# Performance work log

Measured on AMD Instinct MI355X. Metric: run time of the kernel, lower is better.

## Reference

```python
import jax, jax.numpy as jnp
import numpy as np

EMBED_DIM = 1024
NUM_HEADS = 16
HEAD_DIM = EMBED_DIM // NUM_HEADS
SCALING = HEAD_DIM ** -0.5
NEG_FILL = -1e30


def setup_inputs() -> dict:
    key = jax.random.key(0)
    k1, k2, k3 = jax.random.split(key, 3)
    T, B, E = 2048, 4, EMBED_DIM
    query = jax.random.normal(k1, (T, B, E), dtype=jnp.float32)
    key_padding_mask = jnp.zeros((B, T), dtype=bool)  # 1 = padded key
    # xavier_uniform-like init
    lim_in = (6.0 / (3 * E + E)) ** 0.5
    in_proj_weight = jax.random.uniform(k2, (3 * E, E), minval=-lim_in, maxval=lim_in, dtype=jnp.float32)
    in_proj_bias = jnp.zeros((3 * E,), dtype=jnp.float32)
    lim_out = (6.0 / (E + E)) ** 0.5
    out_w = jax.random.uniform(k3, (E, E), minval=-lim_out, maxval=lim_out, dtype=jnp.float32)
    out_b = jnp.zeros((E,), dtype=jnp.float32)
    return {"query": query, "key_padding_mask": key_padding_mask,
            "in_proj_weight": in_proj_weight, "in_proj_bias": in_proj_bias,
            "out_w": out_w, "out_b": out_b}


def reference(query, key_padding_mask, in_proj_weight, in_proj_bias, out_w, out_b):
    T, B, E = query.shape
    H, D = NUM_HEADS, HEAD_DIM
    # fused in-projection (self-attention: qkv from same input)
    qkv = query @ in_proj_weight.T + in_proj_bias  # [T,B,3E]
    q, k, v = jnp.split(qkv, 3, axis=-1)
    q = q * SCALING
    q = q.reshape(T, B, H, D)
    k = k.reshape(T, B, H, D)
    v = v.reshape(T, B, H, D)
    # attention scores [B,H,T,S]
    scores = jnp.einsum('tbhd,sbhd->bhts', q, k)
    scores = jnp.where(key_padding_mask[:, None, None, :], NEG_FILL, scores)
    attn_w = jax.nn.softmax(scores, axis=-1)  # [B,H,T,S]
    # weighted sum of values -> [T,B,E]
    attn = jnp.einsum('bhts,sbhd->tbhd', attn_w, v).reshape(T, B, E)
    attn = attn @ out_w.T + out_b
    attn_w_avg = jnp.sum(attn_w, axis=1) / H  # [B,T,S]
    return attn, attn_w_avg
```

## Files before the change

### kernel.cpp

```cpp
#include <hip/hip_runtime.h>
#include <stdint.h>

#define QSCALE 0.18033688011112042f

typedef unsigned short u16;
typedef unsigned int u32;
typedef unsigned long long u64;
typedef _Float16 f16;
typedef __attribute__((ext_vector_type(2))) __fp16 h16x2;
typedef __attribute__((ext_vector_type(8))) _Float16 f16x8;
typedef __attribute__((ext_vector_type(8))) __bf16 bf16x8;
typedef __attribute__((ext_vector_type(4))) float f32x4;
typedef __attribute__((ext_vector_type(16))) float f32x16;
typedef __attribute__((ext_vector_type(8))) u16 u16x8;
typedef __attribute__((ext_vector_type(4))) u32 u32x4;

__device__ __forceinline__ void gl_lds16(const void* g, void* l) {
  __builtin_amdgcn_global_load_lds(
      (const __attribute__((address_space(1))) void*)g,
      (__attribute__((address_space(3))) void*)l, 16, 0, 0);
}

__device__ __forceinline__ u16 f2bf(float f) {
  unsigned int u = __float_as_uint(f);
  u += 0x7FFFu + ((u >> 16) & 1u);
  return (u16)(u >> 16);
}

extern "C" __global__ __launch_bounds__(256) void cvt_all(
    const float* __restrict__ query, const float* __restrict__ w_in,
    const float* __restrict__ w_out, u16* __restrict__ dst) {
  int i = (blockIdx.x * 256 + threadIdx.x) * 4;
  const float* src;
  int off;
  if (i < 8388608) {
    src = query; off = i;
  } else if (i < 11534336) {
    src = w_in; off = i - 8388608;
  } else {
    src = w_out; off = i - 11534336;
  }
  float4 v = *(const float4*)(src + off);
  ushort4 o;
  o.x = f2bf(v.x); o.y = f2bf(v.y); o.z = f2bf(v.z); o.w = f2bf(v.w);
  *(ushort4*)(dst + i) = o;
}

extern "C" __global__ __launch_bounds__(128) void mask_bits(
    const unsigned char* __restrict__ mask, u64* __restrict__ mbits) {
  const int i = threadIdx.x;
  const unsigned char* p = mask + i * 64;
  u64 bits = 0;
#pragma unroll
  for (int j = 0; j < 8; ++j) {
    const u64 c = *(const u64*)(p + j * 8);
#pragma unroll
    for (int bb = 0; bb < 8; ++bb)
      if ((c >> (8 * bb)) & 0xFFull) bits |= 1ull << (j * 8 + bb);
  }
  mbits[i] = bits;
}

extern "C" __global__ __launch_bounds__(256) void gemm_qkv(
    const u16* __restrict__ X, const u16* __restrict__ W,
    const float* __restrict__ bias,
    u16* __restrict__ qb, u16* __restrict__ kb, u16* __restrict__ vb) {
  const int tid = threadIdx.x;
  const int w = tid >> 6, lane = tid & 63;
  const int lg = lane >> 4, ll = lane & 15;
  const int wm = w >> 1, wn = w & 1;
  const int row0A = blockIdx.x * 128;
  const int row0B = blockIdx.y * 128;

  __shared__ __align__(16) u16 As[2][128 * 32];
  __shared__ __align__(16) u16 Bs[2][128 * 32];

  f32x4 acc[4][4] = {};

  const int r_st = tid >> 2;
  const int cb_st = (tid & 3) * 16;

#pragma unroll
  for (int it = 0; it < 2; ++it) {
    gl_lds16((const char*)X + ((size_t)(row0A + it * 64 + r_st) * 1024) * 2 + cb_st,
             (char*)&As[0][0] + it * 4096 + w * 1024);
    gl_lds16((const char*)W + ((size_t)(row0B + it * 64 + r_st) * 1024) * 2 + cb_st,
             (char*)&Bs[0][0] + it * 4096 + w * 1024);
  }

  for (int kt = 0; kt < 32; ++kt) {
    const int cur = kt & 1;
    asm volatile("s_waitcnt vmcnt(0)" ::: "memory");
    __syncthreads();
    if (kt + 1 < 32) {
      const int k0 = (kt + 1) * 32;
#pragma unroll
      for (int it = 0; it < 2; ++it) {
        gl_lds16((const char*)X + ((size_t)(row0A + it * 64 + r_st) * 1024 + k0) * 2 + cb_st,
                 (char*)&As[cur ^ 1][0] + it * 4096 + w * 1024);
        gl_lds16((const char*)W + ((size_t)(row0B + it * 64 + r_st) * 1024 + k0) * 2 + cb_st,
                 (char*)&Bs[cur ^ 1][0] + it * 4096 + w * 1024);
      }
    }
    const u16* Ab = &As[cur][0];
    const u16* Bb = &Bs[cur][0];
    const int kc = lg * 8;
    bf16x8 a[4], bfr[4];
#pragma unroll
    for (int i = 0; i < 4; ++i)
      a[i] = *(const bf16x8*)(Ab + (wm * 64 + i * 16 + ll) * 32 + kc);
#pragma unroll
    for (int j = 0; j < 4; ++j)
      bfr[j] = *(const bf16x8*)(Bb + (wn * 64 + j * 16 + ll) * 32 + kc);
#pragma unroll
    for (int i = 0; i < 4; ++i)
#pragma unroll
      for (int j = 0; j < 4; ++j)
        acc[i][j] = __builtin_amdgcn_mfma_f32_16x16x32_bf16(a[i], bfr[j], acc[i][j], 0, 0, 0);
  }

  const int which = row0B >> 10;
  if (which == 2) {
#pragma unroll
    for (int j = 0; j < 4; ++j) {
      const int n = row0B + wn * 64 + j * 16 + ll;
      const float bv = bias[n];
      const int n2 = n & 1023;
      const int hh = n2 >> 6, dd = n2 & 63;
#pragma unroll
      for (int i = 0; i < 4; ++i)
#pragma unroll
        for (int r = 0; r < 4; ++r) {
          const int m = row0A + wm * 64 + i * 16 + lg * 4 + r;
          const int tt = m >> 2, bb = m & 3;
          const f16 hv = (f16)(acc[i][j][r] + bv);
          vb[((size_t)(bb * 16 + hh) * 2048 + tt) * 64 + dd] =
              __builtin_bit_cast(u16, hv);
        }
    }
  } else {
    u16* dst = which == 0 ? qb : kb;
    const float scl = which == 0 ? QSCALE : 1.0f;
#pragma unroll
    for (int j = 0; j < 4; ++j) {
      const int n = row0B + wn * 64 + j * 16 + ll;
      const float bv = bias[n];
      const int n2 = n & 1023;
      const int hh = n2 >> 6, dd = n2 & 63;
#pragma unroll
      for (int i = 0; i < 4; ++i)
#pragma unroll
        for (int r = 0; r < 4; ++r) {
          const int m = row0A + wm * 64 + i * 16 + lg * 4 + r;
          const int tt = m >> 2, bb = m & 3;
          dst[((size_t)(bb * 16 + hh) * 2048 + tt) * 64 + dd] =
              f2bf((acc[i][j][r] + bv) * scl);
        }
    }
  }
}

extern "C" __global__ __launch_bounds__(256) void transpose_v(
    const u16* __restrict__ v, u16* __restrict__ vt) {
  const int blk = blockIdx.x;
  const int bh = blk >> 5, tt = blk & 31;
  const int t0 = tt * 64;
  const int tid = threadIdx.x;
  __shared__ __align__(16) u16 tile[64][72];
  const u16* src = v + ((size_t)bh * 2048 + t0) * 64;
#pragma unroll
  for (int it = 0; it < 2; ++it) {
    const int r = it * 32 + (tid >> 3);
    const int c = (tid & 7) * 8;
    *(u16x8*)(&tile[r][c]) = *(const u16x8*)(src + (size_t)r * 64 + c);
  }
  __syncthreads();
  u16* dstb = vt + (size_t)bh * 64 * 2048 + t0;
#pragma unroll
  for (int it = 0; it < 2; ++it) {
    const int d = it * 32 + (tid >> 3);
    const int s = (tid & 7) * 8;
    u16x8 o;
#pragma unroll
    for (int jj = 0; jj < 8; ++jj) o[jj] = tile[s + jj][d];
    *(u16x8*)(dstb + (size_t)d * 2048 + s) = o;
  }
}

extern "C" __global__ __launch_bounds__(256, 4) void flash_fwd(
    const u16* __restrict__ q, const u16* __restrict__ k,
    const u16* __restrict__ vt, const u64* __restrict__ mbits,
    u16* __restrict__ attn_pre, float* __restrict__ stat_il) {
  const int lb = ((blockIdx.x & 7) << 7) + (blockIdx.x >> 3);
  const int bh = lb >> 4, tt = lb & 15;
  const int b = bh >> 4, hd = bh & 15;
  const int t0 = tt * 128;
  const int tid = threadIdx.x, w = tid >> 6, lane = tid & 63;
  const int hl = lane >> 5;
  const int l31 = lane & 31;

  __shared__ __align__(16) u16 Ks[2][64 * 64];
  __shared__ __align__(16) u16 Vs[2][64 * 64];

  const int qrow = t0 + w * 32 + l31;
  const u16* qp = q + ((size_t)bh * 2048 + qrow) * 64 + hl * 8;
  bf16x8 qreg[4];
#pragma unroll
  for (int kg = 0; kg < 4; ++kg) qreg[kg] = *(const bf16x8*)(qp + kg * 16);

  f32x16 po[2] = {};
  float ls0 = 0.f, ls1 = 0.f;
  const h16x2 ones = {(__fp16)1.0f, (__fp16)1.0f};

  const int slot_r = tid >> 3;
  const int slot_c8 = (tid & 7) ^ (slot_r & 7);

#define STAGE_F(buf, s0_)                                                      \
  do {                                                                         \
    _Pragma("unroll") for (int it2 = 0; it2 < 2; ++it2) {                      \
      const int rr = it2 * 32 + slot_r;                                        \
      gl_lds16((const char*)k +                                                \
                   (((size_t)bh * 2048 + (s0_) + rr) * 64 + slot_c8 * 8) * 2,  \
               (char*)&Ks[buf][0] + it2 * 4096 + w * 1024);                    \
      gl_lds16((const char*)vt +                                               \
                   (((size_t)bh * 64 + rr) * 2048 + (s0_) + slot_c8 * 8) * 2,  \
               (char*)&Vs[buf][0] + it2 * 4096 + w * 1024);                    \
    }                                                                          \
  } while (0)

  STAGE_F(0, 0);
  asm volatile("s_waitcnt vmcnt(0)" ::: "memory");
  __builtin_amdgcn_s_barrier();

  for (int t = 0; t < 32; ++t) {
    const u64 mb = mbits[b * 32 + t];
    const int cur = t & 1;
    if (t + 1 < 32) STAGE_F(cur ^ 1, (t + 1) * 64);

    const char* Kb = (const char*)&Ks[cur][0];
    const char* Vb = (const char*)&Vs[cur][0];

#pragma unroll
    for (int kt = 0; kt < 2; ++kt) {
      f32x16 z = {};
      const int key = kt * 32 + l31;
      __builtin_amdgcn_s_setprio(1);
#pragma unroll
      for (int kg = 0; kg < 4; ++kg) {
        const bf16x8 kf = *(const bf16x8*)(
            Kb + key * 128 + ((((kg << 1) | hl) ^ (key & 7)) << 4));
        z = __builtin_amdgcn_mfma_f32_32x32x16_bf16(kf, qreg[kg], z, 0, 0, 0);
      }
      __builtin_amdgcn_s_setprio(0);

      float ps[16];
#pragma unroll
      for (int r = 0; r < 16; ++r) ps[r] = __builtin_amdgcn_exp2f(z[r]);
      const u32 m32 = (u32)(mb >> (kt * 32));
      if (m32) {
#pragma unroll
        for (int r = 0; r < 16; ++r) {
          const int bitpos = (r & 3) + 8 * (r >> 2) + 4 * hl;
          if ((m32 >> bitpos) & 1u) ps[r] = 0.f;
        }
      }

      u32 w8[8];
#pragma unroll
      for (int j = 0; j < 8; ++j) {
        const h16x2 pk = __builtin_amdgcn_cvt_pkrtz(ps[2 * j], ps[2 * j + 1]);
        w8[j] = __builtin_bit_cast(u32, pk);
        if (j & 1)
          ls1 = __builtin_amdgcn_fdot2(pk, ones, ls1, false);
        else
          ls0 = __builtin_amdgcn_fdot2(pk, ones, ls0, false);
      }

#pragma unroll
      for (int f = 0; f < 2; ++f) {
        u32 d0 = w8[4 * f], d1 = w8[4 * f + 1];
        u32 s0w = w8[4 * f + 2], s1w = w8[4 * f + 3];
        asm volatile("v_permlane32_swap_b32 %0, %1" : "+v"(d0), "+v"(s0w));
        asm volatile("v_permlane32_swap_b32 %0, %1" : "+v"(d1), "+v"(s1w));
        const f16x8 pa = __builtin_bit_cast(f16x8, (u32x4){d0, d1, s0w, s1w});
        const int g = kt * 2 + f;
        __builtin_amdgcn_s_setprio(1);
#pragma unroll
        for (int dt = 0; dt < 2; ++dt) {
          const int d = dt * 32 + l31;
          const f16x8 vf = *(const f16x8*)(
              Vb + d * 128 + ((((g << 1) | hl) ^ (d & 7)) << 4));
          po[dt] = __builtin_amdgcn_mfma_f32_32x32x16_f16(pa, vf, po[dt], 0, 0, 0);
        }
        __builtin_amdgcn_s_setprio(0);
      }
    }

    asm volatile("s_waitcnt vmcnt(0)" ::: "memory");
    __builtin_amdgcn_s_barrier();
  }

  float lsum = ls0 + ls1;
  lsum += __shfl_xor(lsum, 32, 64);
  const float linv = 1.0f / lsum;
  if (lane < 32)
    stat_il[(size_t)bh * 2048 + t0 + w * 32 + lane] = linv;

#pragma unroll
  for (int r = 0; r < 16; ++r) {
    const int qi = (r & 3) + 8 * (r >> 2) + 4 * hl;
    const float lv = __shfl(linv, qi, 64);
    const int trow = t0 + w * 32 + qi;
#pragma unroll
    for (int dt = 0; dt < 2; ++dt) {
      const int dd = dt * 32 + l31;
      attn_pre[((size_t)(trow * 4 + b)) * 1024 + hd * 64 + dd] =
          f2bf(po[dt][r] * lv);
    }
  }
#undef STAGE_F
}

extern "C" __global__ __launch_bounds__(256, 3) void wavg(
    const u16* __restrict__ q, const u16* __restrict__ k,
    const u64* __restrict__ mbits,
    const float* __restrict__ stat_il, float* __restrict__ wout) {
  const int lb = ((blockIdx.x & 7) << 8) + (blockIdx.x >> 3);
  const int b = lb >> 9, tt = (lb >> 5) & 15, st = lb & 31;
  const int t0 = tt * 128, s0 = st * 64;
  const int tid = threadIdx.x, w = tid >> 6, lane = tid & 63;
  const int hl = lane >> 5;
  const int l31 = lane & 31;

  __shared__ __align__(16) u16 Qs[2][128 * 64];
  __shared__ __align__(16) u16 Ks2[2][64 * 64];

  const int slot_r8 = tid >> 3;
  const int slot_c8 = (tid & 7) ^ (slot_r8 & 7);

  const u64 mbw = mbits[b * 32 + st];
  const u32 m32lo = (u32)mbw, m32hi = (u32)(mbw >> 32);
  const bool domask = mbw != 0ull;

#define STAGE_W(buf, hh)                                                       \
  do {                                                                         \
    const size_t qo_ = (size_t)(b * 16 + (hh)) * 2048;                         \
    _Pragma("unroll") for (int i2 = 0; i2 < 4; ++i2) {                         \
      const int rr = i2 * 32 + slot_r8;                                        \
      gl_lds16((const char*)q + ((qo_ + t0 + rr) * 64 + slot_c8 * 8) * 2,      \
               (char*)&Qs[buf][0] + i2 * 4096 + w * 1024);                     \
    }                                                                          \
    _Pragma("unroll") for (int i2 = 0; i2 < 2; ++i2) {                         \
      const int rr = i2 * 32 + slot_r8;                                        \
      gl_lds16((const char*)k + ((qo_ + s0 + rr) * 64 + slot_c8 * 8) * 2,      \
               (char*)&Ks2[buf][0] + i2 * 4096 + w * 1024);                    \
    }                                                                          \
  } while (0)

  STAGE_W(0, 0);
  asm volatile("s_waitcnt vmcnt(0)" ::: "memory");
  __syncthreads();

  float accw[32] = {};
  for (int h = 0; h < 16; ++h) {
    const int cur = h & 1;
    const float ilh =
        stat_il[(size_t)(b * 16 + h) * 2048 + t0 + w * 32 + l31];

    if (h + 1 < 16) STAGE_W(cur ^ 1, h + 1);

    const char* Qb = (const char*)&Qs[cur][0];
    const char* Kb = (const char*)&Ks2[cur][0];

    const int qr = w * 32 + l31;
    bf16x8 qf[4];
#pragma unroll
    for (int kg = 0; kg < 4; ++kg)
      qf[kg] = *(const bf16x8*)(
          Qb + qr * 128 + ((((kg << 1) | hl) ^ (qr & 7)) << 4));

    f32x16 z0 = {}, z1 = {};
    __builtin_amdgcn_s_setprio(1);
#pragma unroll
    for (int kg = 0; kg < 4; ++kg) {
      const int key = l31;
      const bf16x8 kf = *(const bf16x8*)(
          Kb + key * 128 + ((((kg << 1) | hl) ^ (key & 7)) << 4));
      z0 = __builtin_amdgcn_mfma_f32_32x32x16_bf16(kf, qf[kg], z0, 0, 0, 0);
    }
#pragma unroll
    for (int kg = 0; kg < 4; ++kg) {
      const int key = 32 + l31;
      const bf16x8 kf = *(const bf16x8*)(
          Kb + key * 128 + ((((kg << 1) | hl) ^ (key & 7)) << 4));
      z1 = __builtin_amdgcn_mfma_f32_32x32x16_bf16(kf, qf[kg], z1, 0, 0, 0);
    }
    __builtin_amdgcn_s_setprio(0);

#pragma unroll
    for (int r = 0; r < 16; ++r) {
      float p = __builtin_amdgcn_exp2f(z0[r]);
      if (domask) {
        const int bitpos = (r & 3) + 8 * (r >> 2) + 4 * hl;
        if ((m32lo >> bitpos) & 1u) p = 0.f;
      }
      accw[r] = fmaf(p, ilh, accw[r]);
    }
#pragma unroll
    for (int r = 0; r < 16; ++r) {
      float p = __builtin_amdgcn_exp2f(z1[r]);
      if (domask) {
        const int bitpos = (r & 3) + 8 * (r >> 2) + 4 * hl;
        if ((m32hi >> bitpos) & 1u) p = 0.f;
      }
      accw[16 + r] = fmaf(p, ilh, accw[16 + r]);
    }

    asm volatile("s_waitcnt vmcnt(0)" ::: "memory");
    __syncthreads();
  }

  float* tb = ((float*)&Qs[0][0]) + w * 2048;
#pragma unroll
  for (int kt = 0; kt < 2; ++kt)
#pragma unroll
    for (int j = 0; j < 4; ++j) {
      f32x4 qd;
#pragma unroll
      for (int e = 0; e < 4; ++e) qd[e] = accw[kt * 16 + 4 * j + e] * 0.0625f;
      const int slot = kt * 8 + 2 * j + hl;
      *(f32x4*)(tb + l31 * 64 + ((slot ^ (l31 & 7)) << 2)) = qd;
    }
  __syncthreads();
#pragma unroll
  for (int j2 = 0; j2 < 8; ++j2) {
    const int row = j2 * 4 + (lane >> 4);
    const int slot = lane & 15;
    const f32x4 v = *(const f32x4*)(tb + row * 64 + ((slot ^ (row & 7)) << 2));
    *(f32x4*)(wout + ((size_t)b * 2048 + t0 + w * 32 + row) * 2048 + s0 +
              slot * 4) = v;
  }
#undef STAGE_W
}

extern "C" __global__ __launch_bounds__(256) void gemm_out(
    const u16* __restrict__ A, const u16* __restrict__ W,
    const float* __restrict__ bias, float* __restrict__ out) {
  const int tid = threadIdx.x;
  const int w = tid >> 6, lane = tid & 63;
  const int lg = lane >> 4, ll = lane & 15;
  const int wm = w >> 1, wn = w & 1;
  const int row0A = blockIdx.x * 128;
  const int row0B = blockIdx.y * 128;

  __shared__ __align__(16) u16 As[2][128 * 32];
  __shared__ __align__(16) u16 Bs[2][128 * 32];

  f32x4 acc[4][4] = {};
  const int r_st = tid >> 2;
  const int cb_st = (tid & 3) * 16;

#pragma unroll
  for (int it = 0; it < 2; ++it) {
    gl_lds16((const char*)A + ((size_t)(row0A + it * 64 + r_st) * 1024) * 2 + cb_st,
             (char*)&As[0][0] + it * 4096 + w * 1024);
    gl_lds16((const char*)W + ((size_t)(row0B + it * 64 + r_st) * 1024) * 2 + cb_st,
             (char*)&Bs[0][0] + it * 4096 + w * 1024);
  }

  for (int kt = 0; kt < 32; ++kt) {
    const int cur = kt & 1;
    asm volatile("s_waitcnt vmcnt(0)" ::: "memory");
    __syncthreads();
    if (kt + 1 < 32) {
      const int k0 = (kt + 1) * 32;
#pragma unroll
      for (int it = 0; it < 2; ++it) {
        gl_lds16((const char*)A + ((size_t)(row0A + it * 64 + r_st) * 1024 + k0) * 2 + cb_st,
                 (char*)&As[cur ^ 1][0] + it * 4096 + w * 1024);
        gl_lds16((const char*)W + ((size_t)(row0B + it * 64 + r_st) * 1024 + k0) * 2 + cb_st,
                 (char*)&Bs[cur ^ 1][0] + it * 4096 + w * 1024);
      }
    }
    const u16* Ab = &As[cur][0];
    const u16* Bb = &Bs[cur][0];
    const int kc = lg * 8;
    bf16x8 a[4], bfr[4];
#pragma unroll
    for (int i = 0; i < 4; ++i)
      a[i] = *(const bf16x8*)(Ab + (wm * 64 + i * 16 + ll) * 32 + kc);
#pragma unroll
    for (int j = 0; j < 4; ++j)
      bfr[j] = *(const bf16x8*)(Bb + (wn * 64 + j * 16 + ll) * 32 + kc);
#pragma unroll
    for (int i = 0; i < 4; ++i)
#pragma unroll
      for (int j = 0; j < 4; ++j)
        acc[i][j] = __builtin_amdgcn_mfma_f32_16x16x32_bf16(a[i], bfr[j], acc[i][j], 0, 0, 0);
  }

#pragma unroll
  for (int j = 0; j < 4; ++j) {
    const int n = row0B + wn * 64 + j * 16 + ll;
    const float bv = bias[n];
#pragma unroll
    for (int i = 0; i < 4; ++i)
#pragma unroll
      for (int r = 0; r < 4; ++r) {
        const int m = row0A + wm * 64 + i * 16 + lg * 4 + r;
        out[(size_t)m * 1024 + n] = acc[i][j][r] + bv;
      }
  }
}

extern "C" void kernel_launch(void* const* d_in, const int* in_sizes, int n_in,
                              void* d_out, int out_size, void* d_ws, size_t ws_size,
                              hipStream_t stream) {
  const float* query = (const float*)d_in[0];
  const unsigned char* mask = (const unsigned char*)d_in[1];
  const float* w_in = (const float*)d_in[2];
  const float* b_in = (const float*)d_in[3];
  const float* w_out = (const float*)d_in[4];
  const float* b_out = (const float*)d_in[5];

  float* out0 = (float*)d_out;
  float* outw = out0 + (size_t)8388608;

  char* ws = (char*)d_ws;
  u16* Xbf   = (u16*)(ws + 0);
  u16* Wqkv  = (u16*)(ws + 16777216);
  u16* Woutb = (u16*)(ws + 23068672);
  u16* qb    = (u16*)(ws + 25165824);
  u16* kb    = (u16*)(ws + 41943040);
  u16* vb    = (u16*)(ws + 58720256);
  u16* vtb   = (u16*)(ws + 75497472);
  u16* ap    = (u16*)(ws + 92274688);
  float* sil = (float*)(ws + 109051904);
  u64* mbits = (u64*)(ws + 109576192);

  cvt_all<<<12288, 256, 0, stream>>>(query, w_in, w_out, Xbf);
  mask_bits<<<1, 128, 0, stream>>>(mask, mbits);
  gemm_qkv<<<dim3(64, 24), 256, 0, stream>>>(Xbf, Wqkv, b_in, qb, kb, vb);
  transpose_v<<<2048, 256, 0, stream>>>(vb, vtb);
  flash_fwd<<<1024, 256, 0, stream>>>(qb, kb, vtb, mbits, ap, sil);
  wavg<<<2048, 256, 0, stream>>>(qb, kb, mbits, sil, outw);
  gemm_out<<<dim3(64, 8), 256, 0, stream>>>(ap, Woutb, b_out, out0);
}
```

Measured before the change: 290.8 us.

## Enlarge QKV GEMM tiles to 256x256x64 with swizzled LDS and interleaved prefetch

Rewrites the QKV projection GEMM to use 512-thread blocks computing 256x256 output tiles with a K-step of 64 instead of 128x128x32. The LDS layout is XOR-swizzled to avoid bank conflicts, the next-stage global-to-LDS loads are spread across the MFMA sub-steps, and MFMA sections are run at raised wave priority. This raises arithmetic intensity and cuts barrier count. In exchange it uses 128KB of LDS and more accumulator registers per block, and the grid shrinks to 384 blocks, which may limit occupancy and wave-level parallelism.

```diff
diff --git a/kernel.cpp b/kernel.cpp
--- a/kernel.cpp
+++ b/kernel.cpp
@@ -61,63 +61,87 @@
   mbits[i] = bits;
 }
 
-extern "C" __global__ __launch_bounds__(256) void gemm_qkv(
+extern "C" __global__ __launch_bounds__(512, 2) void gemm_qkv(
     const u16* __restrict__ X, const u16* __restrict__ W,
     const float* __restrict__ bias,
     u16* __restrict__ qb, u16* __restrict__ kb, u16* __restrict__ vb) {
   const int tid = threadIdx.x;
   const int w = tid >> 6, lane = tid & 63;
   const int lg = lane >> 4, ll = lane & 15;
-  const int wm = w >> 1, wn = w & 1;
-  const int row0A = blockIdx.x * 128;
-  const int row0B = blockIdx.y * 128;
-
-  __shared__ __align__(16) u16 As[2][128 * 32];
-  __shared__ __align__(16) u16 Bs[2][128 * 32];
-
-  f32x4 acc[4][4] = {};
-
-  const int r_st = tid >> 2;
-  const int cb_st = (tid & 3) * 16;
-
-#pragma unroll
-  for (int it = 0; it < 2; ++it) {
-    gl_lds16((const char*)X + ((size_t)(row0A + it * 64 + r_st) * 1024) * 2 + cb_st,
-             (char*)&As[0][0] + it * 4096 + w * 1024);
-    gl_lds16((const char*)W + ((size_t)(row0B + it * 64 + r_st) * 1024) * 2 + cb_st,
-             (char*)&Bs[0][0] + it * 4096 + w * 1024);
-  }
-
-  for (int kt = 0; kt < 32; ++kt) {
+  const int wm = w >> 2, wn = w & 3;
+  const int row0A = blockIdx.x * 256;
+  const int row0B = blockIdx.y * 256;
+
+  __shared__ __align__(16) u16 As[2][256 * 64];
+  __shared__ __align__(16) u16 Bs[2][256 * 64];
+
+  f32x4 acc[8][4] = {};
+
+  const int s_row = tid >> 3;
+  const int g_slot = (tid & 7) ^ (s_row & 7);
+
+#define STAGE_PART(mat, kt_, lds, i)                                           \
+  gl_lds16((const char*)(mat) +                                                \
+               ((size_t)(((mat) == X ? row0A : row0B) + (i)*64 + s_row) * 1024 \
+                + (kt_)*64 + g_slot * 8) * 2,                                  \
+           (char*)&lds[0] + (i)*8192 + w * 1024)
+
+#pragma unroll
+  for (int i = 0; i < 4; ++i) {
+    STAGE_PART(X, 0, As[0], i);
+    STAGE_PART(W, 0, Bs[0], i);
+  }
+  asm volatile("s_waitcnt vmcnt(0)" ::: "memory");
+  __builtin_amdgcn_s_barrier();
+
+  for (int kt = 0; kt < 16; ++kt) {
     const int cur = kt & 1;
+    const char* Ab = (const char*)&As[cur][0];
+    const char* Bb = (const char*)&Bs[cur][0];
+
+    bf16x8 bfr[4][2];
+#pragma unroll
+    for (int j = 0; j < 4; ++j) {
+      const int brow = wn * 64 + j * 16 + ll;
+#pragma unroll
+      for (int ks = 0; ks < 2; ++ks)
+        bfr[j][ks] = *(const bf16x8*)(
+            Bb + brow * 128 + (((ks * 4 + lg) ^ (brow & 7)) << 4));
+    }
+
+#pragma unroll
+    for (int p = 0; p < 4; ++p) {
+      if (kt + 1 < 16) {
+        if (p & 1) STAGE_PART(W, kt + 1, Bs[cur ^ 1], (p >> 1) * 2 + 0),
+                   STAGE_PART(W, kt + 1, Bs[cur ^ 1], (p >> 1) * 2 + 1);
+        else       STAGE_PART(X, kt + 1, As[cur ^ 1], (p >> 1) * 2 + 0),
+                   STAGE_PART(X, kt + 1, As[cur ^ 1], (p >> 1) * 2 + 1);
+      }
+      bf16x8 a[2][2];
+#pragma unroll
+      for (int i2 = 0; i2 < 2; ++i2) {
+        const int arow = wm * 128 + (p * 2 + i2) * 16 + ll;
+#pragma unroll
+        for (int ks = 0; ks < 2; ++ks)
+          a[i2][ks] = *(const bf16x8*)(
+              Ab + arow * 128 + (((ks * 4 + lg) ^ (arow & 7)) << 4));
+      }
+      __builtin_amdgcn_s_setprio(1);
+#pragma unroll
+      for (int i2 = 0; i2 < 2; ++i2)
+#pragma unroll
+        for (int j = 0; j < 4; ++j)
+#pragma unroll
+          for (int ks = 0; ks < 2; ++ks)
+            acc[p * 2 + i2][j] = __builtin_amdgcn_mfma_f32_16x16x32_bf16(
+                a[i2][ks], bfr[j][ks], acc[p * 2 + i2][j], 0, 0, 0);
+      __builtin_amdgcn_s_setprio(0);
+    }
+
     asm volatile("s_waitcnt vmcnt(0)" ::: "memory");
-    __syncthreads();
-    if (kt + 1 < 32) {
-      const int k0 = (kt + 1) * 32;
-#pragma unroll
-      for (int it = 0; it < 2; ++it) {
-        gl_lds16((const char*)X + ((size_t)(row0A + it * 64 + r_st) * 1024 + k0) * 2 + cb_st,
-                 (char*)&As[cur ^ 1][0] + it * 4096 + w * 1024);
-        gl_lds16((const char*)W + ((size_t)(row0B + it * 64 + r_st) * 1024 + k0) * 2 + cb_st,
-                 (char*)&Bs[cur ^ 1][0] + it * 4096 + w * 1024);
-      }
-    }
-    const u16* Ab = &As[cur][0];
-    const u16* Bb = &Bs[cur][0];
-    const int kc = lg * 8;
-    bf16x8 a[4], bfr[4];
-#pragma unroll
-    for (int i = 0; i < 4; ++i)
-      a[i] = *(const bf16x8*)(Ab + (wm * 64 + i * 16 + ll) * 32 + kc);
-#pragma unroll
-    for (int j = 0; j < 4; ++j)
-      bfr[j] = *(const bf16x8*)(Bb + (wn * 64 + j * 16 + ll) * 32 + kc);
-#pragma unroll
-    for (int i = 0; i < 4; ++i)
-#pragma unroll
-      for (int j = 0; j < 4; ++j)
-        acc[i][j] = __builtin_amdgcn_mfma_f32_16x16x32_bf16(a[i], bfr[j], acc[i][j], 0, 0, 0);
-  }
+    __builtin_amdgcn_s_barrier();
+  }
+#undef STAGE_PART
 
   const int which = row0B >> 10;
   if (which == 2) {
@@ -128,10 +152,10 @@
       const int n2 = n & 1023;
       const int hh = n2 >> 6, dd = n2 & 63;
 #pragma unroll
-      for (int i = 0; i < 4; ++i)
+      for (int i = 0; i < 8; ++i)
 #pragma unroll
         for (int r = 0; r < 4; ++r) {
-          const int m = row0A + wm * 64 + i * 16 + lg * 4 + r;
+          const int m = row0A + wm * 128 + i * 16 + lg * 4 + r;
           const int tt = m >> 2, bb = m & 3;
           const f16 hv = (f16)(acc[i][j][r] + bv);
           vb[((size_t)(bb * 16 + hh) * 2048 + tt) * 64 + dd] =
@@ -148,10 +172,10 @@
       const int n2 = n & 1023;
       const int hh = n2 >> 6, dd = n2 & 63;
 #pragma unroll
-      for (int i = 0; i < 4; ++i)
+      for (int i = 0; i < 8; ++i)
 #pragma unroll
         for (int r = 0; r < 4; ++r) {
-          const int m = row0A + wm * 64 + i * 16 + lg * 4 + r;
+          const int m = row0A + wm * 128 + i * 16 + lg * 4 + r;
           const int tt = m >> 2, bb = m & 3;
           dst[((size_t)(bb * 16 + hh) * 2048 + tt) * 64 + dd] =
               f2bf((acc[i][j][r] + bv) * scl);
@@ -540,7 +564,7 @@
 
   cvt_all<<<12288, 256, 0, stream>>>(query, w_in, w_out, Xbf);
   mask_bits<<<1, 128, 0, stream>>>(mask, mbits);
-  gemm_qkv<<<dim3(64, 24), 256, 0, stream>>>(Xbf, Wqkv, b_in, qb, kb, vb);
+  gemm_qkv<<<dim3(32, 12), 512, 0, stream>>>(Xbf, Wqkv, b_in, qb, kb, vb);
   transpose_v<<<2048, 256, 0, stream>>>(vb, vtb);
   flash_fwd<<<1024, 256, 0, stream>>>(qb, kb, vtb, mbits, ap, sil);
   wavg<<<2048, 256, 0, stream>>>(qb, kb, mbits, sil, outw);
```

After: 292.6 us. No clear change (+0.6%).

## Stage QKV GEMM epilogue through LDS and fuse V transpose into it

Applied to the files above, without the earlier changes.

The QKV GEMM epilogue now writes results into a swizzled shared-memory tile and then issues 16-byte vectorized global stores for Q and K, replacing scattered 2-byte stores. For V, the transposed layout is produced directly from the LDS tile, which removes the separate transpose_v kernel along with its extra global write and read of V. In exchange the epilogue gains an extra barrier, shared-memory traffic, and register pressure from the 32-element column buffer.

```diff
diff --git a/kernel.cpp b/kernel.cpp
--- a/kernel.cpp
+++ b/kernel.cpp
@@ -64,7 +64,7 @@
 extern "C" __global__ __launch_bounds__(256) void gemm_qkv(
     const u16* __restrict__ X, const u16* __restrict__ W,
     const float* __restrict__ bias,
-    u16* __restrict__ qb, u16* __restrict__ kb, u16* __restrict__ vb) {
+    u16* __restrict__ qb, u16* __restrict__ kb, u16* __restrict__ vtb) {
   const int tid = threadIdx.x;
   const int w = tid >> 6, lane = tid & 63;
   const int lg = lane >> 4, ll = lane & 15;
@@ -72,8 +72,9 @@
   const int row0A = blockIdx.x * 128;
   const int row0B = blockIdx.y * 128;
 
-  __shared__ __align__(16) u16 As[2][128 * 32];
-  __shared__ __align__(16) u16 Bs[2][128 * 32];
+  __shared__ __align__(16) u16 SM[16384];
+  u16* Asb = SM;
+  u16* Bsb = SM + 8192;
 
   f32x4 acc[4][4] = {};
 
@@ -83,9 +84,9 @@
 #pragma unroll
   for (int it = 0; it < 2; ++it) {
     gl_lds16((const char*)X + ((size_t)(row0A + it * 64 + r_st) * 1024) * 2 + cb_st,
-             (char*)&As[0][0] + it * 4096 + w * 1024);
+             (char*)Asb + it * 4096 + w * 1024);
     gl_lds16((const char*)W + ((size_t)(row0B + it * 64 + r_st) * 1024) * 2 + cb_st,
-             (char*)&Bs[0][0] + it * 4096 + w * 1024);
+             (char*)Bsb + it * 4096 + w * 1024);
   }
 
   for (int kt = 0; kt < 32; ++kt) {
@@ -94,16 +95,17 @@
     __syncthreads();
     if (kt + 1 < 32) {
       const int k0 = (kt + 1) * 32;
+      const int nxt = cur ^ 1;
 #pragma unroll
       for (int it = 0; it < 2; ++it) {
         gl_lds16((const char*)X + ((size_t)(row0A + it * 64 + r_st) * 1024 + k0) * 2 + cb_st,
-                 (char*)&As[cur ^ 1][0] + it * 4096 + w * 1024);
+                 (char*)(Asb + nxt * 4096) + it * 4096 + w * 1024);
         gl_lds16((const char*)W + ((size_t)(row0B + it * 64 + r_st) * 1024 + k0) * 2 + cb_st,
-                 (char*)&Bs[cur ^ 1][0] + it * 4096 + w * 1024);
-      }
-    }
-    const u16* Ab = &As[cur][0];
-    const u16* Bb = &Bs[cur][0];
+                 (char*)(Bsb + nxt * 4096) + it * 4096 + w * 1024);
+      }
+    }
+    const u16* Ab = Asb + cur * 4096;
+    const u16* Bb = Bsb + cur * 4096;
     const int kc = lg * 8;
     bf16x8 a[4], bfr[4];
 #pragma unroll
@@ -119,71 +121,62 @@
         acc[i][j] = __builtin_amdgcn_mfma_f32_16x16x32_bf16(a[i], bfr[j], acc[i][j], 0, 0, 0);
   }
 
+  __syncthreads();
   const int which = row0B >> 10;
-  if (which == 2) {
-#pragma unroll
-    for (int j = 0; j < 4; ++j) {
-      const int n = row0B + wn * 64 + j * 16 + ll;
-      const float bv = bias[n];
-      const int n2 = n & 1023;
-      const int hh = n2 >> 6, dd = n2 & 63;
-#pragma unroll
-      for (int i = 0; i < 4; ++i)
-#pragma unroll
-        for (int r = 0; r < 4; ++r) {
-          const int m = row0A + wm * 64 + i * 16 + lg * 4 + r;
-          const int tt = m >> 2, bb = m & 3;
-          const f16 hv = (f16)(acc[i][j][r] + bv);
-          vb[((size_t)(bb * 16 + hh) * 2048 + tt) * 64 + dd] =
-              __builtin_bit_cast(u16, hv);
+  const float scl = which == 0 ? QSCALE : 1.0f;
+  const int hh0 = (row0B & 1023) >> 6;
+
+#pragma unroll
+  for (int j = 0; j < 4; ++j) {
+    const int n = row0B + wn * 64 + j * 16 + ll;
+    const float bv = bias[n];
+#pragma unroll
+    for (int i = 0; i < 4; ++i)
+#pragma unroll
+      for (int r = 0; r < 4; ++r) {
+        const float val = (acc[i][j][r] + bv) * scl;
+        u16 pay;
+        if (which == 2) {
+          const f16 hv = (f16)val;
+          pay = __builtin_bit_cast(u16, hv);
+        } else {
+          pay = f2bf(val);
         }
-    }
+        const int lrow = wn * 128 + r * 32 + wm * 16 + i * 4 + lg;
+        const int slot = (j * 2 + (ll >> 3)) ^ (lrow & 7);
+        SM[lrow * 64 + slot * 8 + (ll & 7)] = pay;
+      }
+  }
+  __syncthreads();
+
+  if (which < 2) {
+    u16* dst = which ? kb : qb;
+    const int lrow = tid;
+    const int hh = hh0 + (lrow >> 7);
+    const int bb = (lrow >> 5) & 3;
+    const int tt = (row0A >> 2) + (lrow & 31);
+    u16* gp = dst + ((size_t)(bb * 16 + hh) * 2048 + tt) * 64;
+#pragma unroll
+    for (int s = 0; s < 8; ++s)
+      *(u16x8*)(gp + s * 8) = *(const u16x8*)(SM + lrow * 64 + ((s ^ (lrow & 7)) << 3));
   } else {
-    u16* dst = which == 0 ? qb : kb;
-    const float scl = which == 0 ? QSCALE : 1.0f;
-#pragma unroll
-    for (int j = 0; j < 4; ++j) {
-      const int n = row0B + wn * 64 + j * 16 + ll;
-      const float bv = bias[n];
-      const int n2 = n & 1023;
-      const int hh = n2 >> 6, dd = n2 & 63;
-#pragma unroll
-      for (int i = 0; i < 4; ++i)
-#pragma unroll
-        for (int r = 0; r < 4; ++r) {
-          const int m = row0A + wm * 64 + i * 16 + lg * 4 + r;
-          const int tt = m >> 2, bb = m & 3;
-          dst[((size_t)(bb * 16 + hh) * 2048 + tt) * 64 + dd] =
-              f2bf((acc[i][j][r] + bv) * scl);
-        }
-    }
-  }
-}
-
-extern "C" __global__ __launch_bounds__(256) void transpose_v(
-    const u16* __restrict__ v, u16* __restrict__ vt) {
-  const int blk = blockIdx.x;
-  const int bh = blk >> 5, tt = blk & 31;
-  const int t0 = tt * 64;
-  const int tid = threadIdx.x;
-  __shared__ __align__(16) u16 tile[64][72];
-  const u16* src = v + ((size_t)bh * 2048 + t0) * 64;
-#pragma unroll
-  for (int it = 0; it < 2; ++it) {
-    const int r = it * 32 + (tid >> 3);
-    const int c = (tid & 7) * 8;
-    *(u16x8*)(&tile[r][c]) = *(const u16x8*)(src + (size_t)r * 64 + c);
-  }
-  __syncthreads();
-  u16* dstb = vt + (size_t)bh * 64 * 2048 + t0;
-#pragma unroll
-  for (int it = 0; it < 2; ++it) {
-    const int d = it * 32 + (tid >> 3);
-    const int s = (tid & 7) * 8;
-    u16x8 o;
-#pragma unroll
-    for (int jj = 0; jj < 8; ++jj) o[jj] = tile[s + jj][d];
-    *(u16x8*)(dstb + (size_t)d * 2048 + s) = o;
+#pragma unroll
+    for (int u = 0; u < 2; ++u) {
+      const int rid = u * 256 + tid;
+      const int bb = rid >> 7, hhr = (rid >> 6) & 1, dd = rid & 63;
+      const int hh = hh0 + hhr;
+      const int slot0 = dd >> 3, de = dd & 7;
+      u16 col[32];
+#pragma unroll
+      for (int t2 = 0; t2 < 32; ++t2) {
+        const int lrow = hhr * 128 + bb * 32 + t2;
+        col[t2] = SM[lrow * 64 + ((slot0 ^ (lrow & 7)) << 3) + de];
+      }
+      u16* gp = vtb + ((size_t)(bb * 16 + hh) * 64 + dd) * 2048 + (row0A >> 2);
+#pragma unroll
+      for (int sg = 0; sg < 4; ++sg)
+        *(u16x8*)(gp + sg * 8) = *(const u16x8*)(col + sg * 8);
+    }
   }
 }
 
@@ -532,7 +525,6 @@
   u16* Woutb = (u16*)(ws + 23068672);
   u16* qb    = (u16*)(ws + 25165824);
   u16* kb    = (u16*)(ws + 41943040);
-  u16* vb    = (u16*)(ws + 58720256);
   u16* vtb   = (u16*)(ws + 75497472);
   u16* ap    = (u16*)(ws + 92274688);
   float* sil = (float*)(ws + 109051904);
@@ -540,8 +532,7 @@
 
   cvt_all<<<12288, 256, 0, stream>>>(query, w_in, w_out, Xbf);
   mask_bits<<<1, 128, 0, stream>>>(mask, mbits);
-  gemm_qkv<<<dim3(64, 24), 256, 0, stream>>>(Xbf, Wqkv, b_in, qb, kb, vb);
-  transpose_v<<<2048, 256, 0, stream>>>(vb, vtb);
+  gemm_qkv<<<dim3(64, 24), 256, 0, stream>>>(Xbf, Wqkv, b_in, qb, kb, vtb);
   flash_fwd<<<1024, 256, 0, stream>>>(qb, kb, vtb, mbits, ap, sil);
   wavg<<<2048, 256, 0, stream>>>(qb, kb, mbits, sil, outw);
   gemm_out<<<dim3(64, 8), 256, 0, stream>>>(ap, Woutb, b_out, out0);
```

Measured after the change: 286.3 us. Within noise of the previous version (-1.5%).
